# Optimization experiments

Measured on AMD Instinct MI355X. Metric: run time of the kernel, lower is better.

The kernel has to match this reference:

```python
import jax, jax.numpy as jnp
import numpy as np

B, T, D_MODEL = 1, 2048, 4096
NUM_Q_HEADS, NUM_KV_HEADS, KEY_SIZE = 32, 8, 128
ATTN_MULT = 0.08838834764831845  # 1/sqrt(key_size)
MAX_ATTN_VAL = 30.0


def rotate_half(x):
    x1, x2 = jnp.split(x, 2, axis=-1)
    return jnp.concatenate((-x2, x1), axis=-1)


def apply_rope(x):
    # x: [b, t, h, d]; offset = 0, positions = arange(t)
    b, t, h, d = x.shape
    exponents = jnp.arange(0, d, 2, dtype=jnp.float32)
    inv_freq = 1.0 / (10000.0 ** (exponents / d))            # [d/2]
    pos = jnp.arange(t, dtype=jnp.float32)                   # [t]
    phase = pos[:, None] * inv_freq[None, :]                 # [t, d/2]
    phase = jnp.tile(phase, (1, 2))[None, :, None, :]        # [1, t, 1, d] (tiled, not interleaved)
    return (x * jnp.cos(phase) + rotate_half(x) * jnp.sin(phase)).astype(x.dtype)


def setup_inputs() -> dict:
    key = jax.random.key(0)
    ks = jax.random.split(key, 8)
    query = jax.random.normal(ks[0], (B, T, D_MODEL), dtype=jnp.float32)
    kk = jax.random.normal(ks[1], (B, T, D_MODEL), dtype=jnp.float32)
    vv = jax.random.normal(ks[2], (B, T, D_MODEL), dtype=jnp.float32)
    mask = jnp.tril(jnp.ones((T, T), dtype=bool))[None, None, :, :]  # causal [1,1,T,T]
    s = 0.02
    Wq = jax.random.normal(ks[3], (D_MODEL, NUM_Q_HEADS * KEY_SIZE), dtype=jnp.float32) * s
    Wk = jax.random.normal(ks[4], (D_MODEL, NUM_KV_HEADS * KEY_SIZE), dtype=jnp.float32) * s
    Wv = jax.random.normal(ks[5], (D_MODEL, NUM_KV_HEADS * KEY_SIZE), dtype=jnp.float32) * s
    Wo = jax.random.normal(ks[6], (NUM_Q_HEADS * KEY_SIZE, D_MODEL), dtype=jnp.float32) * s
    return {"query": query, "key": kk, "value": vv, "mask": mask,
            "Wq": Wq, "Wk": Wk, "Wv": Wv, "Wo": Wo}


def reference(query, key, value, mask, Wq, Wk, Wv, Wo):
    b, t, _ = query.shape
    d = KEY_SIZE
    h, kv_h = NUM_Q_HEADS, NUM_KV_HEADS
    g = h // kv_h
    # projections (no bias)
    q = (query @ Wq).reshape(b, t, h, d)
    k = (key @ Wk).reshape(b, t, kv_h, d)
    v = (value @ Wv).reshape(b, t, kv_h, d)
    # RoPE on q and k
    q = apply_rope(q)
    k = apply_rope(k)
    # GQA grouping: [b, t, kv_h, g, d]
    q = q.reshape(b, t, kv_h, g, d)
    logits = jnp.einsum('btkgd,bTkd->bkgtT', q, k).astype(jnp.float32)
    logits = logits * ATTN_MULT
    logits = MAX_ATTN_VAL * jnp.tanh(logits / MAX_ATTN_VAL)  # soft-capping
    m = mask[:, :, None, :, :]  # [b,1,1,t,T]
    logits = jnp.where(m, logits, -1e30)
    weights = jax.nn.softmax(logits, axis=-1).astype(query.dtype)
    attn = jnp.einsum('bkgtT,bTkd->btkgd', weights, v)
    attn = attn.reshape(b, t, h * d)
    return attn @ Wo
```

## Files before the change

kernel.cpp:

```cpp
#include <hip/hip_runtime.h>
#include <hip/hip_bf16.h>
#include <stdint.h>
#include <stddef.h>

#define T_SEQ 2048
#define DM    4096
#define NQH   32
#define NKVH  8
#define HD    128
#define ATTN_MULT 0.08838834764831845f

typedef __attribute__((ext_vector_type(8))) short bf16x8;
typedef __attribute__((ext_vector_type(4))) float f32x4;
typedef __attribute__((ext_vector_type(4))) unsigned int u32x4;

__device__ __forceinline__ unsigned short f2b(float f) {
  unsigned u = __builtin_bit_cast(unsigned, f);
  u = u + 0x7FFFu + ((u >> 16) & 1u);
  return (unsigned short)(u >> 16);
}
__device__ __forceinline__ float b2f(unsigned short h) {
  unsigned u = ((unsigned)h) << 16;
  return __builtin_bit_cast(float, u);
}

typedef const __attribute__((address_space(1))) void* gptr1_t;
typedef __attribute__((address_space(3))) void* lptr3_t;
__device__ __forceinline__ void gl_lds16(const void* g, void* l) {
  __builtin_amdgcn_global_load_lds((gptr1_t)g, (lptr3_t)l, 16, 0, 0);
}

__global__ __launch_bounds__(256) void transpose_cast_kernel(
    const float* __restrict__ W, unsigned short* __restrict__ WT, int K, int N) {
  __shared__ float tile[64][65];
  int k0 = blockIdx.x * 64;
  int n0 = blockIdx.y * 64;
  int t = threadIdx.x;
  int rr = t >> 4;
  int cc = t & 15;
#pragma unroll
  for (int c = 0; c < 4; ++c) {
    int row = c * 16 + rr;
    float4 v = *(const float4*)&W[(size_t)(k0 + row) * N + n0 + cc * 4];
    tile[row][cc * 4 + 0] = v.x;
    tile[row][cc * 4 + 1] = v.y;
    tile[row][cc * 4 + 2] = v.z;
    tile[row][cc * 4 + 3] = v.w;
  }
  __syncthreads();
  int orow = t >> 2;
  int kb = (t & 3) * 16;
  u32x4 o1, o2;
#pragma unroll
  for (int u = 0; u < 4; ++u) {
    o1[u] = (unsigned)f2b(tile[kb + 2 * u][orow]) |
            ((unsigned)f2b(tile[kb + 2 * u + 1][orow]) << 16);
    o2[u] = (unsigned)f2b(tile[kb + 8 + 2 * u][orow]) |
            ((unsigned)f2b(tile[kb + 9 + 2 * u][orow]) << 16);
  }
  unsigned short* dst = &WT[(size_t)(n0 + orow) * K + k0 + kb];
  *(u32x4*)dst = o1;
  *(u32x4*)(dst + 8) = o2;
}

__global__ __launch_bounds__(256) void cast3_kernel(
    const float* __restrict__ a0, const float* __restrict__ a1, const float* __restrict__ a2,
    unsigned short* __restrict__ b0, unsigned short* __restrict__ b1, unsigned short* __restrict__ b2) {
  const float* in = blockIdx.z == 0 ? a0 : (blockIdx.z == 1 ? a1 : a2);
  unsigned short* out = blockIdx.z == 0 ? b0 : (blockIdx.z == 1 ? b1 : b2);
  size_t idx = ((size_t)blockIdx.x * 256 + threadIdx.x) * 8;
  float4 x = *(const float4*)(in + idx);
  float4 y = *(const float4*)(in + idx + 4);
  u32x4 v;
  v[0] = (unsigned)f2b(x.x) | ((unsigned)f2b(x.y) << 16);
  v[1] = (unsigned)f2b(x.z) | ((unsigned)f2b(x.w) << 16);
  v[2] = (unsigned)f2b(y.x) | ((unsigned)f2b(y.y) << 16);
  v[3] = (unsigned)f2b(y.z) | ((unsigned)f2b(y.w) << 16);
  *(u32x4*)(out + idx) = v;
}

template <bool F32OUT>
__global__ __launch_bounds__(512, 1) void gemm_dp_kernel(
    const unsigned short* __restrict__ A, const unsigned short* __restrict__ BT,
    void* __restrict__ C, int M, int N, int K) {
  __shared__ unsigned short lds[3 * 24576];

  int nx = gridDim.x;
  int flat = blockIdx.y * nx + blockIdx.x;
  int npx = nx >> 3;
  int xcd = flat & 7, idx = flat >> 3;
  int n0 = (xcd * npx + idx % npx) * 256;
  int m0 = (idx / npx) * 128;

  int t = threadIdx.x;
  int w = t >> 6, l = t & 63;
  int wm = w >> 2, wn = w & 3;
  int lr = l & 15, lh = l >> 4;

  f32x4 acc[4][4] = {};

  int lrow8 = l >> 3;
  int scb = ((l & 7) ^ lrow8) << 4;
  const int NT = K >> 6;

  auto stage = [&](int tt, int bsel) {
    int kb = tt * 64;
#pragma unroll
    for (int c = 0; c < 6; ++c) {
      int chunk = w * 6 + c;
      if (chunk < 16) {
        const char* src = (const char*)A +
            ((size_t)(m0 + chunk * 8 + lrow8) * K + kb) * 2 + scb;
        gl_lds16(src, (char*)lds + bsel * 49152 + chunk * 1024);
      } else {
        const char* src = (const char*)BT +
            ((size_t)(n0 + (chunk - 16) * 8 + lrow8) * K + kb) * 2 + scb;
        gl_lds16(src, (char*)lds + bsel * 49152 + 16384 + (chunk - 16) * 1024);
      }
    }
  };

  stage(0, 0);
  stage(1, 1);
  asm volatile("s_waitcnt vmcnt(6)" ::: "memory");
  __builtin_amdgcn_s_barrier();

  int bsel = 0, bnext = 2;
  for (int tt = 0; tt < NT; ++tt) {
    bool pre = (tt + 2 < NT);
    if (pre) stage(tt + 2, bnext);
    const char* Ab = (const char*)lds + bsel * 49152;
    const char* Bb = Ab + 16384;
#pragma unroll
    for (int ks = 0; ks < 2; ++ks) {
      bf16x8 af[4], bfp[4];
      int cswz = ks * 64;
#pragma unroll
      for (int i = 0; i < 4; ++i) {
        int row = wm * 64 + i * 16 + lr;
        af[i] = *(const bf16x8*)(Ab + row * 128 + ((cswz + lh * 16) ^ ((lr & 7) << 4)));
      }
#pragma unroll
      for (int j = 0; j < 4; ++j) {
        int row = wn * 64 + j * 16 + lr;
        bfp[j] = *(const bf16x8*)(Bb + row * 128 + ((cswz + lh * 16) ^ ((lr & 7) << 4)));
      }
      __builtin_amdgcn_s_setprio(1);
#pragma unroll
      for (int i = 0; i < 4; ++i)
#pragma unroll
        for (int j = 0; j < 4; ++j)
          acc[i][j] = __builtin_amdgcn_mfma_f32_16x16x32_bf16(af[i], bfp[j], acc[i][j], 0, 0, 0);
      __builtin_amdgcn_s_setprio(0);
    }
    if (pre) asm volatile("s_waitcnt vmcnt(6)" ::: "memory");
    else     asm volatile("s_waitcnt vmcnt(0)" ::: "memory");
    __builtin_amdgcn_s_barrier();
    bsel = (bsel == 2) ? 0 : bsel + 1;
    bnext = (bnext == 2) ? 0 : bnext + 1;
  }

#pragma unroll
  for (int i = 0; i < 4; ++i) {
#pragma unroll
    for (int j = 0; j < 4; ++j) {
#pragma unroll
      for (int r = 0; r < 4; ++r) {
        int row = m0 + wm * 64 + i * 16 + lh * 4 + r;
        int col = n0 + wn * 64 + j * 16 + lr;
        if constexpr (F32OUT)
          ((float*)C)[(size_t)row * N + col] = acc[i][j][r];
        else
          ((unsigned short*)C)[(size_t)row * N + col] = f2b(acc[i][j][r]);
      }
    }
  }
}

template <bool F32OUT, bool DUAL>
__global__ __launch_bounds__(256) void gemm_bt_kernel(
    const unsigned short* __restrict__ A0, const unsigned short* __restrict__ B0, void* __restrict__ C0,
    const unsigned short* __restrict__ A1, const unsigned short* __restrict__ B1, void* __restrict__ C1,
    int M, int N, int K) {
  __shared__ unsigned short As[128 * 32];
  __shared__ unsigned short Bs[128 * 32];
  const unsigned short* A = A0;
  const unsigned short* BT = B0;
  void* C = C0;
  if (DUAL && blockIdx.z == 1) { A = A1; BT = B1; C = C1; }

  int nx = gridDim.x;
  int flat = blockIdx.y * nx + blockIdx.x;
  int cpx = (nx * gridDim.y) >> 3;
  int swz = (flat & 7) * cpx + (flat >> 3);
  int m0 = (swz / nx) * 128;
  int n0 = (swz % nx) * 128;

  int t = threadIdx.x;
  int w = t >> 6, l = t & 63;
  int wr = w >> 1, wc = w & 1;
  int lr = l & 15, lh = l >> 4;

  f32x4 acc[4][4] = {};

  int srow0 = (w * 2 + 0) * 16 + (l >> 2);
  int srow1 = (w * 2 + 1) * 16 + (l >> 2);
  int scol = (l & 3) * 8;
  const unsigned short* Aa0 = A + (size_t)(m0 + srow0) * K + scol;
  const unsigned short* Aa1 = A + (size_t)(m0 + srow1) * K + scol;
  const unsigned short* Ba0 = BT + (size_t)(n0 + srow0) * K + scol;
  const unsigned short* Ba1 = BT + (size_t)(n0 + srow1) * K + scol;
  unsigned short* Al0 = &As[(w * 2 + 0) * 512];
  unsigned short* Al1 = &As[(w * 2 + 1) * 512];
  unsigned short* Bl0 = &Bs[(w * 2 + 0) * 512];
  unsigned short* Bl1 = &Bs[(w * 2 + 1) * 512];

  for (int k0 = 0; k0 < K; k0 += 32) {
    gl_lds16(Aa0 + k0, Al0);
    gl_lds16(Aa1 + k0, Al1);
    gl_lds16(Ba0 + k0, Bl0);
    gl_lds16(Ba1 + k0, Bl1);
    __syncthreads();
    bf16x8 af[4], bfr[4];
#pragma unroll
    for (int i = 0; i < 4; ++i)
      af[i] = *(const bf16x8*)&As[(wr * 64 + i * 16 + lr) * 32 + lh * 8];
#pragma unroll
    for (int j = 0; j < 4; ++j)
      bfr[j] = *(const bf16x8*)&Bs[(wc * 64 + j * 16 + lr) * 32 + lh * 8];
#pragma unroll
    for (int i = 0; i < 4; ++i)
#pragma unroll
      for (int j = 0; j < 4; ++j)
        acc[i][j] = __builtin_amdgcn_mfma_f32_16x16x32_bf16(af[i], bfr[j], acc[i][j], 0, 0, 0);
    __syncthreads();
  }

#pragma unroll
  for (int i = 0; i < 4; ++i) {
#pragma unroll
    for (int j = 0; j < 4; ++j) {
#pragma unroll
      for (int r = 0; r < 4; ++r) {
        int row = m0 + wr * 64 + i * 16 + lh * 4 + r;
        int col = n0 + wc * 64 + j * 16 + lr;
        if constexpr (F32OUT)
          ((float*)C)[(size_t)row * N + col] = acc[i][j][r];
        else
          ((unsigned short*)C)[(size_t)row * N + col] = f2b(acc[i][j][r]);
      }
    }
  }
}

__global__ __launch_bounds__(256) void sincos_kernel(float2* __restrict__ tab) {
  int idx = blockIdx.x * 256 + threadIdx.x;
  int i = idx & 63;
  int tpos = idx >> 6;
  float invf = exp2f(-(float)i * (13.287712379549449f / 64.0f));
  float phase = (float)tpos * invf;
  float s, c;
  sincosf(phase, &s, &c);
  tab[idx] = make_float2(c, s);
}

__global__ __launch_bounds__(256) void rope_kernel(unsigned short* __restrict__ X,
                                                   const float2* __restrict__ tab,
                                                   int hshift, float scale) {
  int idx = blockIdx.x * 256 + threadIdx.x;
  int i = idx & 63;
  int rest = idx >> 6;
  int nheads = 1 << hshift;
  int hh = rest & (nheads - 1);
  int tpos = rest >> hshift;
  float2 cs = tab[tpos * 64 + i];
  size_t base = (size_t)tpos * ((size_t)nheads * HD) + (size_t)hh * HD + i;
  float x1 = b2f(X[base]);
  float x2 = b2f(X[base + 64]);
  X[base] = f2b((x1 * cs.x - x2 * cs.y) * scale);
  X[base + 64] = f2b((x2 * cs.x + x1 * cs.y) * scale);
}

__global__ __launch_bounds__(256) void vtrans_kernel(
    const unsigned short* __restrict__ V, unsigned short* __restrict__ VT) {
  size_t flat = ((size_t)blockIdx.x * 256 + threadIdx.x) * 8;
  int t8 = (int)(flat & (T_SEQ - 1));
  int dh = (int)(flat >> 11);
  u32x4 v;
#pragma unroll
  for (int u = 0; u < 4; ++u) {
    unsigned short lo = V[(size_t)(t8 + 2 * u) * (NKVH * HD) + dh];
    unsigned short hi = V[(size_t)(t8 + 2 * u + 1) * (NKVH * HD) + dh];
    v[u] = (unsigned)lo | ((unsigned)hi << 16);
  }
  *(u32x4*)(VT + flat) = v;
}

template <bool DIAG>
__device__ __forceinline__ void softmax_frag(const f32x4 s[4], float& lsum, bf16x8 pf[2],
                                             int lr, int lh, int wq) {
  constexpr float C2f = (float)(-60.0 * 1.4426950408889634);
  float pv[4][4];
#pragma unroll
  for (int ct = 0; ct < 4; ++ct)
#pragma unroll
    for (int r = 0; r < 4; ++r) {
      float u = exp2f(s[ct][r]);
      float p = exp2f(C2f * __builtin_amdgcn_rcpf(u + 1.0f));
      if constexpr (DIAG) {
        int kg = ct * 16 + lh * 4 + r;
        int qg = wq * 16 + lr;
        if (kg > qg) p = 0.0f;
      }
      pv[ct][r] = p;
      lsum += p;
    }
  unsigned pk[4][2];
#pragma unroll
  for (int ct = 0; ct < 4; ++ct) {
    pk[ct][0] = (unsigned)f2b(pv[ct][0]) | ((unsigned)f2b(pv[ct][1]) << 16);
    pk[ct][1] = (unsigned)f2b(pv[ct][2]) | ((unsigned)f2b(pv[ct][3]) << 16);
  }
  int s0 = ((lh & 1) << 5) + lr;
  int s1 = s0 + 16;
  bool hi = (lh >= 2);
#pragma unroll
  for (int ks = 0; ks < 2; ++ks) {
    unsigned a0 = (unsigned)__shfl((int)pk[2 * ks][0], s0, 64);
    unsigned a1 = (unsigned)__shfl((int)pk[2 * ks][1], s0, 64);
    unsigned a2 = (unsigned)__shfl((int)pk[2 * ks][0], s1, 64);
    unsigned a3 = (unsigned)__shfl((int)pk[2 * ks][1], s1, 64);
    unsigned b0 = (unsigned)__shfl((int)pk[2 * ks + 1][0], s0, 64);
    unsigned b1 = (unsigned)__shfl((int)pk[2 * ks + 1][1], s0, 64);
    unsigned b2 = (unsigned)__shfl((int)pk[2 * ks + 1][0], s1, 64);
    unsigned b3 = (unsigned)__shfl((int)pk[2 * ks + 1][1], s1, 64);
    u32x4 f;
    f[0] = hi ? b0 : a0;
    f[1] = hi ? b1 : a1;
    f[2] = hi ? b2 : a2;
    f[3] = hi ? b3 : a3;
    pf[ks] = __builtin_bit_cast(bf16x8, f);
  }
}

template <bool WITHA, bool DIAGA, bool DIAGB>
__device__ __forceinline__ void attn_tile(
    const char* KsCur, const char* VsCur,
    const bf16x8 qfA[4], const bf16x8 qfB[4],
    f32x4 oaccA[8], f32x4 oaccB[8],
    float& lsumA, float& lsumB,
    int lr, int lh, int wq) {
  f32x4 sB[4], sA[4];
#pragma unroll
  for (int ct = 0; ct < 4; ++ct) {
    f32x4 zB = {};
    f32x4 zA = {};
#pragma unroll
    for (int kk = 0; kk < 4; ++kk) {
      int row = ct * 16 + lr;
      int cb = (kk * 32 + lh * 8) * 2;
      bf16x8 kf = *(const bf16x8*)(KsCur + row * 256 + (cb ^ ((row & 7) << 4)));
      zB = __builtin_amdgcn_mfma_f32_16x16x32_bf16(kf, qfB[kk], zB, 0, 0, 0);
      if constexpr (WITHA) zA = __builtin_amdgcn_mfma_f32_16x16x32_bf16(kf, qfA[kk], zA, 0, 0, 0);
    }
    sB[ct] = zB;
    if constexpr (WITHA) sA[ct] = zA;
  }
  bf16x8 pfB[2], pfA[2];
  softmax_frag<DIAGB>(sB, lsumB, pfB, lr, lh, wq);
  if constexpr (WITHA) softmax_frag<DIAGA>(sA, lsumA, pfA, lr, lh, wq);
#pragma unroll
  for (int ks = 0; ks < 2; ++ks) {
    int pcb = (ks * 32 + lh * 8) * 2;
#pragma unroll
    for (int dt = 0; dt < 8; ++dt) {
      int vrow = dt * 16 + lr;
      bf16x8 vf = *(const bf16x8*)(VsCur + ((vrow * 128 + pcb) ^ ((vrow & 7) << 4)));
      oaccB[dt] = __builtin_amdgcn_mfma_f32_16x16x32_bf16(pfB[ks], vf, oaccB[dt], 0, 0, 0);
      if constexpr (WITHA) oaccA[dt] = __builtin_amdgcn_mfma_f32_16x16x32_bf16(pfA[ks], vf, oaccA[dt], 0, 0, 0);
    }
  }
}

__global__ __launch_bounds__(512, 2) void attn_kernel(
    const unsigned short* __restrict__ Q,
    const unsigned short* __restrict__ Kx,
    const unsigned short* __restrict__ VT,
    unsigned short* __restrict__ O) {
  __shared__ unsigned short Ks[2][64 * 128];
  __shared__ unsigned short Vs[2][128 * 64];

  int bx = blockIdx.x;
  int by = blockIdx.y;
  int qtA = bx, qtB = 31 - bx;
  int t = threadIdx.x;
  int w = t >> 6, l = t & 63;
  int wq = w & 3;
  int hh = by * 2 + (w >> 2);
  int kvh = by >> 1;
  int lr = l & 15, lh = l >> 4;

  bf16x8 qfA[4], qfB[4];
  {
    const unsigned short* qpA = Q + (size_t)(qtA * 64 + wq * 16 + lr) * (NQH * HD) + hh * HD + lh * 8;
    const unsigned short* qpB = Q + (size_t)(qtB * 64 + wq * 16 + lr) * (NQH * HD) + hh * HD + lh * 8;
#pragma unroll
    for (int kk = 0; kk < 4; ++kk) {
      qfA[kk] = *(const bf16x8*)(qpA + kk * 32);
      qfB[kk] = *(const bf16x8*)(qpB + kk * 32);
    }
  }

  f32x4 oaccA[8] = {}, oaccB[8] = {};
  float lsumA = 0.f, lsumB = 0.f;

  const char* KgB = (const char*)Kx + (size_t)kvh * HD * 2;
  const char* VgB = (const char*)VT + (size_t)kvh * HD * T_SEQ * 2;

  auto stage = [&](int kt, int b) {
#pragma unroll
    for (int c = 0; c < 2; ++c) {
      int chunk = w * 2 + c;
      int p = chunk * 1024 + l * 16;
      {
        int row = p >> 8;
        int cb = p & 255;
        int cbl = cb ^ ((row & 7) << 4);
        gl_lds16(KgB + (size_t)(kt * 64 + row) * (NKVH * HD * 2) + cbl,
                 (char*)Ks[b] + chunk * 1024);
      }
      {
        int row = p >> 7;
        int cb = p & 127;
        int cbl = cb ^ ((row & 7) << 4);
        gl_lds16(VgB + (size_t)row * (T_SEQ * 2) + (size_t)kt * 128 + cbl,
                 (char*)Vs[b] + chunk * 1024);
      }
    }
  };

  stage(0, 0);
  __syncthreads();

  int cur = 0;
  for (int kt = 0; kt <= qtB; ++kt) {
    if (kt < qtB) stage(kt + 1, cur ^ 1);
    const char* Kc = (const char*)Ks[cur];
    const char* Vc = (const char*)Vs[cur];
    if (kt < qtA)
      attn_tile<true, false, false>(Kc, Vc, qfA, qfB, oaccA, oaccB, lsumA, lsumB, lr, lh, wq);
    else if (kt == qtA)
      attn_tile<true, true, false>(Kc, Vc, qfA, qfB, oaccA, oaccB, lsumA, lsumB, lr, lh, wq);
    else if (kt < qtB)
      attn_tile<false, false, false>(Kc, Vc, qfA, qfB, oaccA, oaccB, lsumA, lsumB, lr, lh, wq);
    else
      attn_tile<false, false, true>(Kc, Vc, qfA, qfB, oaccA, oaccB, lsumA, lsumB, lr, lh, wq);
    __syncthreads();
    cur ^= 1;
  }

  lsumB += __shfl_xor(lsumB, 16, 64);
  lsumB += __shfl_xor(lsumB, 32, 64);
  lsumA += __shfl_xor(lsumA, 16, 64);
  lsumA += __shfl_xor(lsumA, 32, 64);

#pragma unroll
  for (int i = 0; i < 4; ++i) {
    int srcl = (l & 48) | (lh * 4 + i);
    float invB = 1.0f / __shfl(lsumB, srcl, 64);
    float invA = 1.0f / __shfl(lsumA, srcl, 64);
    int qgB = qtB * 64 + wq * 16 + lh * 4 + i;
    int qgA = qtA * 64 + wq * 16 + lh * 4 + i;
#pragma unroll
    for (int dt = 0; dt < 8; ++dt) {
      O[(size_t)qgB * (NQH * HD) + hh * HD + dt * 16 + lr] = f2b(oaccB[dt][i] * invB);
      O[(size_t)qgA * (NQH * HD) + hh * HD + dt * 16 + lr] = f2b(oaccA[dt][i] * invA);
    }
  }
}

extern "C" void kernel_launch(void* const* d_in, const int* in_sizes, int n_in,
                              void* d_out, int out_size, void* d_ws, size_t ws_size,
                              hipStream_t stream) {
  const float* query = (const float*)d_in[0];
  const float* key = (const float*)d_in[1];
  const float* value = (const float*)d_in[2];
  const float* Wq = (const float*)d_in[4];
  const float* Wk = (const float*)d_in[5];
  const float* Wv = (const float*)d_in[6];
  const float* Wo = (const float*)d_in[7];
  float* out = (float*)d_out;

  char* ws = (char*)d_ws;
  constexpr size_t OFF_WQT = 0;
  constexpr size_t OFF_WOT = 33554432;
  constexpr size_t OFF_WKT = 67108864;
  constexpr size_t OFF_WVT = 75497472;
  constexpr size_t OFF_QB = 83886080;
  constexpr size_t OFF_KB = 100663296;
  constexpr size_t OFF_VB = 117440512;
  constexpr size_t OFF_QP = 134217728;
  constexpr size_t OFF_KP = 150994944;
  constexpr size_t OFF_VP = 155189248;
  constexpr size_t OFF_VT = 159383552;
  constexpr size_t OFF_AT = 163577856;
  constexpr size_t WS_NEED = 180355072;
  if (ws_size < WS_NEED) return;

  unsigned short* WqT = (unsigned short*)(ws + OFF_WQT);
  unsigned short* WoT = (unsigned short*)(ws + OFF_WOT);
  unsigned short* WkT = (unsigned short*)(ws + OFF_WKT);
  unsigned short* WvT = (unsigned short*)(ws + OFF_WVT);
  unsigned short* qb = (unsigned short*)(ws + OFF_QB);
  unsigned short* kb = (unsigned short*)(ws + OFF_KB);
  unsigned short* vb = (unsigned short*)(ws + OFF_VB);
  unsigned short* Qp = (unsigned short*)(ws + OFF_QP);
  unsigned short* Kp = (unsigned short*)(ws + OFF_KP);
  unsigned short* Vp = (unsigned short*)(ws + OFF_VP);
  unsigned short* VTb = (unsigned short*)(ws + OFF_VT);
  unsigned short* attnb = (unsigned short*)(ws + OFF_AT);
  float2* tab = (float2*)(ws + OFF_QB);

  transpose_cast_kernel<<<dim3(64, 64), 256, 0, stream>>>(Wq, WqT, DM, NQH * HD);
  transpose_cast_kernel<<<dim3(64, 16), 256, 0, stream>>>(Wk, WkT, DM, NKVH * HD);
  transpose_cast_kernel<<<dim3(64, 16), 256, 0, stream>>>(Wv, WvT, DM, NKVH * HD);
  transpose_cast_kernel<<<dim3(64, 64), 256, 0, stream>>>(Wo, WoT, NQH * HD, DM);
  cast3_kernel<<<dim3(4096, 1, 3), 256, 0, stream>>>(query, key, value, qb, kb, vb);
  gemm_dp_kernel<false><<<dim3(16, 16), 512, 0, stream>>>(
      qb, WqT, Qp, T_SEQ, NQH * HD, DM);
  gemm_bt_kernel<false, true><<<dim3(8, 16, 2), 256, 0, stream>>>(
      kb, WkT, Kp, vb, WvT, Vp, T_SEQ, NKVH * HD, DM);
  sincos_kernel<<<dim3(T_SEQ * 64 / 256), 256, 0, stream>>>(tab);
  constexpr float C1 = (float)(0.08838834764831845 * 1.4426950408889634 / 15.0);
  rope_kernel<<<dim3(T_SEQ * NQH * 64 / 256), 256, 0, stream>>>(Qp, tab, 5, C1);
  rope_kernel<<<dim3(T_SEQ * NKVH * 64 / 256), 256, 0, stream>>>(Kp, tab, 3, 1.0f);
  vtrans_kernel<<<dim3(NKVH * HD * T_SEQ / (256 * 8)), 256, 0, stream>>>(Vp, VTb);
  attn_kernel<<<dim3(16, 16), 512, 0, stream>>>(Qp, Kp, VTb, attnb);
  gemm_dp_kernel<true><<<dim3(16, 16), 512, 0, stream>>>(
      attnb, WoT, out, T_SEQ, DM, DM);
}
```

Measured before the change: 433.3 us.

## Fuse Q, K and V projections into one grouped high-throughput GEMM launch

Replaces the separate Q-projection launch and the smaller-tile dual K/V GEMM with a single grouped kernel of 384 blocks. It reuses the LDS-pipelined 128x256 GEMM body for all three projections. This removes one launch and the tail gap between them, and moves K/V onto the faster tiled path. Blocks 256 and up map to K or V tiles without XCD swizzling, so cache locality for those tiles may be weaker.

Measured after the change: 400.9 us. -7.5%, faster.

```diff
diff --git a/kernel.cpp b/kernel.cpp
--- a/kernel.cpp
+++ b/kernel.cpp
@@ -80,18 +80,10 @@
 }
 
 template <bool F32OUT>
-__global__ __launch_bounds__(512, 1) void gemm_dp_kernel(
+__device__ __forceinline__ void gemm_dp_body(
+    unsigned short* lds,
     const unsigned short* __restrict__ A, const unsigned short* __restrict__ BT,
-    void* __restrict__ C, int M, int N, int K) {
-  __shared__ unsigned short lds[3 * 24576];
-
-  int nx = gridDim.x;
-  int flat = blockIdx.y * nx + blockIdx.x;
-  int npx = nx >> 3;
-  int xcd = flat & 7, idx = flat >> 3;
-  int n0 = (xcd * npx + idx % npx) * 256;
-  int m0 = (idx / npx) * 128;
-
+    void* __restrict__ C, int N, int K, int m0, int n0) {
   int t = threadIdx.x;
   int w = t >> 6, l = t & 63;
   int wm = w >> 2, wn = w & 3;
@@ -177,80 +169,45 @@
   }
 }
 
-template <bool F32OUT, bool DUAL>
-__global__ __launch_bounds__(256) void gemm_bt_kernel(
-    const unsigned short* __restrict__ A0, const unsigned short* __restrict__ B0, void* __restrict__ C0,
-    const unsigned short* __restrict__ A1, const unsigned short* __restrict__ B1, void* __restrict__ C1,
-    int M, int N, int K) {
-  __shared__ unsigned short As[128 * 32];
-  __shared__ unsigned short Bs[128 * 32];
-  const unsigned short* A = A0;
-  const unsigned short* BT = B0;
-  void* C = C0;
-  if (DUAL && blockIdx.z == 1) { A = A1; BT = B1; C = C1; }
-
+__global__ __launch_bounds__(512, 1) void qkv_dp_kernel(
+    const unsigned short* __restrict__ qb, const unsigned short* __restrict__ WqT, unsigned short* __restrict__ Qp,
+    const unsigned short* __restrict__ kb, const unsigned short* __restrict__ WkT, unsigned short* __restrict__ Kp,
+    const unsigned short* __restrict__ vb, const unsigned short* __restrict__ WvT, unsigned short* __restrict__ Vp) {
+  __shared__ unsigned short lds[3 * 24576];
+  int flat = blockIdx.x;
+  const unsigned short *A, *BT;
+  unsigned short* C;
+  int N, m0, n0;
+  if (flat < 256) {
+    A = qb; BT = WqT; C = Qp; N = NQH * HD;
+    int xcd = flat & 7, idx = flat >> 3;
+    n0 = (xcd * 2 + (idx & 1)) * 256;
+    m0 = (idx >> 1) * 128;
+  } else {
+    int lf = flat - 256;
+    int sel = lf >> 6;
+    int local = lf & 63;
+    A = sel ? vb : kb;
+    BT = sel ? WvT : WkT;
+    C = sel ? Vp : Kp;
+    N = NKVH * HD;
+    m0 = (local >> 2) * 128;
+    n0 = (local & 3) * 256;
+  }
+  gemm_dp_body<false>(lds, A, BT, C, N, DM, m0, n0);
+}
+
+__global__ __launch_bounds__(512, 1) void gemm_dp_kernel(
+    const unsigned short* __restrict__ A, const unsigned short* __restrict__ BT,
+    float* __restrict__ C, int M, int N, int K) {
+  __shared__ unsigned short lds[3 * 24576];
   int nx = gridDim.x;
   int flat = blockIdx.y * nx + blockIdx.x;
-  int cpx = (nx * gridDim.y) >> 3;
-  int swz = (flat & 7) * cpx + (flat >> 3);
-  int m0 = (swz / nx) * 128;
-  int n0 = (swz % nx) * 128;
-
-  int t = threadIdx.x;
-  int w = t >> 6, l = t & 63;
-  int wr = w >> 1, wc = w & 1;
-  int lr = l & 15, lh = l >> 4;
-
-  f32x4 acc[4][4] = {};
-
-  int srow0 = (w * 2 + 0) * 16 + (l >> 2);
-  int srow1 = (w * 2 + 1) * 16 + (l >> 2);
-  int scol = (l & 3) * 8;
-  const unsigned short* Aa0 = A + (size_t)(m0 + srow0) * K + scol;
-  const unsigned short* Aa1 = A + (size_t)(m0 + srow1) * K + scol;
-  const unsigned short* Ba0 = BT + (size_t)(n0 + srow0) * K + scol;
-  const unsigned short* Ba1 = BT + (size_t)(n0 + srow1) * K + scol;
-  unsigned short* Al0 = &As[(w * 2 + 0) * 512];
-  unsigned short* Al1 = &As[(w * 2 + 1) * 512];
-  unsigned short* Bl0 = &Bs[(w * 2 + 0) * 512];
-  unsigned short* Bl1 = &Bs[(w * 2 + 1) * 512];
-
-  for (int k0 = 0; k0 < K; k0 += 32) {
-    gl_lds16(Aa0 + k0, Al0);
-    gl_lds16(Aa1 + k0, Al1);
-    gl_lds16(Ba0 + k0, Bl0);
-    gl_lds16(Ba1 + k0, Bl1);
-    __syncthreads();
-    bf16x8 af[4], bfr[4];
-#pragma unroll
-    for (int i = 0; i < 4; ++i)
-      af[i] = *(const bf16x8*)&As[(wr * 64 + i * 16 + lr) * 32 + lh * 8];
-#pragma unroll
-    for (int j = 0; j < 4; ++j)
-      bfr[j] = *(const bf16x8*)&Bs[(wc * 64 + j * 16 + lr) * 32 + lh * 8];
-#pragma unroll
-    for (int i = 0; i < 4; ++i)
-#pragma unroll
-      for (int j = 0; j < 4; ++j)
-        acc[i][j] = __builtin_amdgcn_mfma_f32_16x16x32_bf16(af[i], bfr[j], acc[i][j], 0, 0, 0);
-    __syncthreads();
-  }
-
-#pragma unroll
-  for (int i = 0; i < 4; ++i) {
-#pragma unroll
-    for (int j = 0; j < 4; ++j) {
-#pragma unroll
-      for (int r = 0; r < 4; ++r) {
-        int row = m0 + wr * 64 + i * 16 + lh * 4 + r;
-        int col = n0 + wc * 64 + j * 16 + lr;
-        if constexpr (F32OUT)
-          ((float*)C)[(size_t)row * N + col] = acc[i][j][r];
-        else
-          ((unsigned short*)C)[(size_t)row * N + col] = f2b(acc[i][j][r]);
-      }
-    }
-  }
+  int npx = nx >> 3;
+  int xcd = flat & 7, idx = flat >> 3;
+  int n0 = (xcd * npx + idx % npx) * 256;
+  int m0 = (idx / npx) * 128;
+  gemm_dp_body<true>(lds, A, BT, C, N, K, m0, n0);
 }
 
 __global__ __launch_bounds__(256) void sincos_kernel(float2* __restrict__ tab) {
@@ -526,16 +483,12 @@
   transpose_cast_kernel<<<dim3(64, 16), 256, 0, stream>>>(Wv, WvT, DM, NKVH * HD);
   transpose_cast_kernel<<<dim3(64, 64), 256, 0, stream>>>(Wo, WoT, NQH * HD, DM);
   cast3_kernel<<<dim3(4096, 1, 3), 256, 0, stream>>>(query, key, value, qb, kb, vb);
-  gemm_dp_kernel<false><<<dim3(16, 16), 512, 0, stream>>>(
-      qb, WqT, Qp, T_SEQ, NQH * HD, DM);
-  gemm_bt_kernel<false, true><<<dim3(8, 16, 2), 256, 0, stream>>>(
-      kb, WkT, Kp, vb, WvT, Vp, T_SEQ, NKVH * HD, DM);
+  qkv_dp_kernel<<<dim3(384), 512, 0, stream>>>(qb, WqT, Qp, kb, WkT, Kp, vb, WvT, Vp);
   sincos_kernel<<<dim3(T_SEQ * 64 / 256), 256, 0, stream>>>(tab);
   constexpr float C1 = (float)(0.08838834764831845 * 1.4426950408889634 / 15.0);
   rope_kernel<<<dim3(T_SEQ * NQH * 64 / 256), 256, 0, stream>>>(Qp, tab, 5, C1);
   rope_kernel<<<dim3(T_SEQ * NKVH * 64 / 256), 256, 0, stream>>>(Kp, tab, 3, 1.0f);
   vtrans_kernel<<<dim3(NKVH * HD * T_SEQ / (256 * 8)), 256, 0, stream>>>(Vp, VTb);
   attn_kernel<<<dim3(16, 16), 512, 0, stream>>>(Qp, Kp, VTb, attnb);
-  gemm_dp_kernel<true><<<dim3(16, 16), 512, 0, stream>>>(
-      attnb, WoT, out, T_SEQ, DM, DM);
-}
+  gemm_dp_kernel<<<dim3(16, 16), 512, 0, stream>>>(attnb, WoT, out, T_SEQ, DM, DM);
+}
```
